# Optimization experiments

Measured on AMD Instinct MI355X. Metric: run time of the kernel, lower is better.

Reference implementation:

```python
import jax, jax.numpy as jnp
import numpy as np

H = 1024
V = 50257
S = 20


def setup_inputs() -> dict:
    key = jax.random.key(0)
    ks = jax.random.split(key, 13)
    sc = 0.02
    return {
        "token": jax.random.randint(ks[0], (1,), 0, V),
        "hidden": jax.random.normal(ks[1], (1, 1, H), jnp.float32),
        "encoder_outputs": jax.random.normal(ks[2], (S, 1, H), jnp.float32),
        "embed_table": jax.random.normal(ks[3], (V, H), jnp.float32) * sc,
        "attn_w": jax.random.normal(ks[4], (H, 2 * H), jnp.float32) * sc,
        "attn_b": jax.random.normal(ks[5], (H,), jnp.float32) * sc,
        "v_w": jax.random.normal(ks[6], (1, H), jnp.float32) * sc,
        "gru_w_ih": jax.random.normal(ks[7], (3 * H, 2 * H), jnp.float32) * sc,
        "gru_w_hh": jax.random.normal(ks[8], (3 * H, H), jnp.float32) * sc,
        "gru_b_ih": jax.random.normal(ks[9], (3 * H,), jnp.float32) * sc,
        "gru_b_hh": jax.random.normal(ks[10], (3 * H,), jnp.float32) * sc,
        "out_w": jax.random.normal(ks[11], (V, H), jnp.float32) * sc,
        "out_b": jax.random.normal(ks[12], (V,), jnp.float32) * sc,
    }


def reference(token, hidden, encoder_outputs, embed_table, attn_w, attn_b, v_w,
              gru_w_ih, gru_w_hh, gru_b_ih, gru_b_hh, out_w, out_b):
    s = encoder_outputs.shape[0]
    # embedding lookup -> [1,1,H]
    embed = embed_table[token].reshape(1, 1, -1)
    enc = jnp.transpose(encoder_outputs, (1, 0, 2))  # [1,S,H]
    h_rep = jnp.broadcast_to(hidden, (1, s, hidden.shape[-1]))  # repeat over src_len
    # Bahdanau additive attention
    energy = jnp.tanh(jnp.concatenate([h_rep, enc], axis=2) @ attn_w.T + attn_b)  # [1,S,H]
    scores = jnp.squeeze(energy @ v_w.T, axis=2)  # [1,S]
    attn = jax.nn.softmax(scores, axis=1)[:, None, :]  # [1,1,S]
    weighted = jnp.einsum('bqs,bsh->bqh', attn, enc)  # [1,1,H]
    # single-step GRU (PyTorch gate layout: r,z,n)
    x = jnp.concatenate([embed, weighted], axis=2)[0]  # [1,2H]
    h0 = hidden[0]  # [1,H]
    gi = x @ gru_w_ih.T + gru_b_ih  # [1,3H]
    gh = h0 @ gru_w_hh.T + gru_b_hh  # [1,3H]
    i_r, i_z, i_n = jnp.split(gi, 3, axis=1)
    h_r, h_z, h_n = jnp.split(gh, 3, axis=1)
    r = jax.nn.sigmoid(i_r + h_r)
    z = jax.nn.sigmoid(i_z + h_z)
    n = jnp.tanh(i_n + r * h_n)
    h_new = (1.0 - z) * n + z * h0  # [1,H]
    prediction = jax.nn.log_softmax(h_new @ out_w.T + out_b, axis=1)  # [1,V]
    return prediction, h_new[None]  # ([1,V], [1,1,H])
```

## Files before the change

### kernel.cpp

```cpp
#include <hip/hip_runtime.h>
#include <math.h>

#define H 1024
#define S 20
#define V 50257
#define NGRP ((V + 3) / 4)
#define KC_BLOCKS 512
#define KC_WAVES (KC_BLOCKS * 8)

__device__ __forceinline__ float wave_reduce_sum(float v) {
  #pragma unroll
  for (int off = 32; off > 0; off >>= 1)
    v += __shfl_xor(v, off, 64);
  return v;
}

__global__ __launch_bounds__(256) void kA(
    const int* __restrict__ token,
    const float* __restrict__ hidden,
    const float* __restrict__ enc,
    const float* __restrict__ embed_table,
    const float* __restrict__ attn_w,
    const float* __restrict__ attn_b,
    const float* __restrict__ v_w,
    const float* __restrict__ w_ih,
    const float* __restrict__ w_hh,
    const float* __restrict__ b_ih,
    const float* __restrict__ b_hh,
    float* __restrict__ bpart,
    float* __restrict__ gie,
    float* __restrict__ Emat,
    float* __restrict__ ghv)
{
  __shared__ float esh[4][S];
  const int t = threadIdx.x;
  const int lane = t & 63;
  const int wv = t >> 6;
  const int b = blockIdx.x;

  if (b < 256) {
    const int j = b * 4 + wv;
    const float* wrow = attn_w + (size_t)j * (2 * H);
    float4 wlo[4], whi[4], hid4[4];
    #pragma unroll
    for (int q = 0; q < 4; ++q) {
      const int idx = lane + 64 * q;
      wlo[q]  = ((const float4*)wrow)[idx];
      whi[q]  = ((const float4*)(wrow + H))[idx];
      hid4[q] = ((const float4*)hidden)[idx];
    }
    float hp = 0.f;
    #pragma unroll
    for (int q = 0; q < 4; ++q)
      hp += wlo[q].x * hid4[q].x + wlo[q].y * hid4[q].y +
            wlo[q].z * hid4[q].z + wlo[q].w * hid4[q].w;
    hp = wave_reduce_sum(hp);

    float myval = 0.f;
    #pragma unroll
    for (int s = 0; s < S; ++s) {
      const float4* e4 = (const float4*)(enc + s * H);
      float es = 0.f;
      #pragma unroll
      for (int q = 0; q < 4; ++q) {
        const float4 e = e4[lane + 64 * q];
        es += whi[q].x * e.x + whi[q].y * e.y + whi[q].z * e.z + whi[q].w * e.w;
      }
      es = wave_reduce_sum(es);
      if (lane == s) myval = es;
    }
    if (lane < S)
      esh[wv][lane] = tanhf(hp + myval + attn_b[j]) * v_w[j];
    __syncthreads();
    if (wv == 0 && lane < S)
      bpart[lane * 256 + b] =
          esh[0][lane] + esh[1][lane] + esh[2][lane] + esh[3][lane];
  } else if (b < 1024) {
    const int W = (b - 256) * 4 + wv;
    const float* wr = w_ih + (size_t)W * (2 * H);
    const float* embed = embed_table + (size_t)(*token) * H;
    float a = 0.f;
    #pragma unroll
    for (int q = 0; q < 4; ++q) {
      const int idx = lane + 64 * q;
      const float4 w = ((const float4*)wr)[idx];
      const float4 e = ((const float4*)embed)[idx];
      a += w.x * e.x + w.y * e.y + w.z * e.z + w.w * e.w;
    }
    a = wave_reduce_sum(a);
    if (lane == 0) gie[W] = a + b_ih[W];
  } else if (b < 1792) {
    const int W = (b - 1024) * 4 + wv;
    const float* wr = w_ih + (size_t)W * (2 * H) + H;
    float4 wv4[4];
    #pragma unroll
    for (int q = 0; q < 4; ++q) wv4[q] = ((const float4*)wr)[lane + 64 * q];
    float myE = 0.f;
    #pragma unroll
    for (int s = 0; s < S; ++s) {
      const float4* e4 = (const float4*)(enc + s * H);
      float es = 0.f;
      #pragma unroll
      for (int q = 0; q < 4; ++q) {
        const float4 e = e4[lane + 64 * q];
        es += wv4[q].x * e.x + wv4[q].y * e.y + wv4[q].z * e.z + wv4[q].w * e.w;
      }
      es = wave_reduce_sum(es);
      if (lane == s) myE = es;
    }
    if (lane < S) Emat[lane * (3 * H) + W] = myE;
  } else {
    const int W = (b - 1792) * 4 + wv;
    const float* wr = w_hh + (size_t)W * H;
    float a = 0.f;
    #pragma unroll
    for (int q = 0; q < 4; ++q) {
      const int idx = lane + 64 * q;
      const float4 w = ((const float4*)wr)[idx];
      const float4 h = ((const float4*)hidden)[idx];
      a += w.x * h.x + w.y * h.y + w.z * h.z + w.w * h.w;
    }
    a = wave_reduce_sum(a);
    if (lane == 0) ghv[W] = a + b_hh[W];
  }
}

__global__ __launch_bounds__(512) void kC(
    const float* __restrict__ bpart,
    const float* __restrict__ gie,
    const float* __restrict__ Emat,
    const float* __restrict__ ghv,
    const float* __restrict__ hidden,
    const float* __restrict__ out_w,
    const float* __restrict__ out_b,
    float* __restrict__ out,
    float* __restrict__ pmax,
    float* __restrict__ psum)
{
  __shared__ float scores_sh[S];
  __shared__ float attn_sh[S];
  __shared__ float hnew_lds[H];
  __shared__ float stat_m[8];
  __shared__ float stat_s[8];
  const int t = threadIdx.x;
  const int lane = t & 63;
  const int wv = t >> 6;
  const int b = blockIdx.x;

  for (int s = wv; s < S; s += 8) {
    const float4 p = ((const float4*)(bpart + s * 256))[lane];
    float v = wave_reduce_sum(p.x + p.y + p.z + p.w);
    if (lane == 0) scores_sh[s] = v;
  }
  __syncthreads();
  if (t == 0) {
    float m = -1e30f;
    for (int s = 0; s < S; ++s) m = fmaxf(m, scores_sh[s]);
    float sum = 0.f;
    for (int s = 0; s < S; ++s) {
      const float e = expf(scores_sh[s] - m);
      attn_sh[s] = e;
      sum += e;
    }
    const float inv = 1.f / sum;
    for (int s = 0; s < S; ++s) attn_sh[s] *= inv;
  }
  __syncthreads();

  #pragma unroll
  for (int r = 0; r < 2; ++r) {
    const int j = t + r * 512;
    float g0 = 0.f, g1 = 0.f, g2 = 0.f;
    #pragma unroll
    for (int s = 0; s < S; ++s) {
      const float a = attn_sh[s];
      const float* Es = Emat + s * (3 * H);
      g0 += a * Es[j];
      g1 += a * Es[H + j];
      g2 += a * Es[2 * H + j];
    }
    const float i_r = gie[j]         + g0;
    const float i_z = gie[H + j]     + g1;
    const float i_n = gie[2 * H + j] + g2;
    const float h_r = ghv[j];
    const float h_z = ghv[H + j];
    const float h_n = ghv[2 * H + j];
    const float rr = 1.f / (1.f + expf(-(i_r + h_r)));
    const float zz = 1.f / (1.f + expf(-(i_z + h_z)));
    const float nn = tanhf(i_n + rr * h_n);
    const float hn = (1.f - zz) * nn + zz * hidden[j];
    hnew_lds[j] = hn;
    if (b == 0) out[V + j] = hn;
  }
  __syncthreads();

  float4 h4[4];
  #pragma unroll
  for (int q = 0; q < 4; ++q)
    h4[q] = ((const float4*)hnew_lds)[lane + 64 * q];

  const int gw = b * 8 + wv;
  float wm = -INFINITY, wsum = 0.f;

  for (int grp = gw; grp < NGRP; grp += KC_WAVES) {
    const int vbase = grp * 4;
    const int v0 = vbase;
    const int v1 = (vbase + 1 < V) ? vbase + 1 : (V - 1);
    const int v2 = (vbase + 2 < V) ? vbase + 2 : (V - 1);
    const int v3 = (vbase + 3 < V) ? vbase + 3 : (V - 1);
    const float4* r0 = (const float4*)(out_w + (size_t)v0 * H);
    const float4* r1 = (const float4*)(out_w + (size_t)v1 * H);
    const float4* r2 = (const float4*)(out_w + (size_t)v2 * H);
    const float4* r3 = (const float4*)(out_w + (size_t)v3 * H);
    float a0 = 0.f, a1 = 0.f, a2 = 0.f, a3 = 0.f;
    #pragma unroll
    for (int q = 0; q < 4; ++q) {
      const int idx = lane + 64 * q;
      const float4 w0 = r0[idx];
      const float4 w1 = r1[idx];
      const float4 w2 = r2[idx];
      const float4 w3 = r3[idx];
      a0 += w0.x * h4[q].x + w0.y * h4[q].y + w0.z * h4[q].z + w0.w * h4[q].w;
      a1 += w1.x * h4[q].x + w1.y * h4[q].y + w1.z * h4[q].z + w1.w * h4[q].w;
      a2 += w2.x * h4[q].x + w2.y * h4[q].y + w2.z * h4[q].z + w2.w * h4[q].w;
      a3 += w3.x * h4[q].x + w3.y * h4[q].y + w3.z * h4[q].z + w3.w * h4[q].w;
    }
    a0 = wave_reduce_sum(a0);
    a1 = wave_reduce_sum(a1);
    a2 = wave_reduce_sum(a2);
    a3 = wave_reduce_sum(a3);
    const float val0 = a0 + out_b[v0];
    const float val1 = (vbase + 1 < V) ? a1 + out_b[v1] : -INFINITY;
    const float val2 = (vbase + 2 < V) ? a2 + out_b[v2] : -INFINITY;
    const float val3 = (vbase + 3 < V) ? a3 + out_b[v3] : -INFINITY;

    if (lane == 0) {
      if (vbase + 3 < V) {
        float4 o; o.x = val0; o.y = val1; o.z = val2; o.w = val3;
        *reinterpret_cast<float4*>(out + vbase) = o;
      } else {
        out[vbase] = val0;
        if (vbase + 1 < V) out[vbase + 1] = val1;
        if (vbase + 2 < V) out[vbase + 2] = val2;
      }
    }

    const float gm = fmaxf(fmaxf(val0, val1), fmaxf(val2, val3));
    const float M2 = fmaxf(wm, gm);
    wsum = wsum * expf(wm - M2) +
           expf(val0 - M2) + expf(val1 - M2) + expf(val2 - M2) + expf(val3 - M2);
    wm = M2;
  }

  if (lane == 0) { stat_m[wv] = wm; stat_s[wv] = wsum; }
  __syncthreads();
  if (t == 0) {
    float M = stat_m[0], Ss = stat_s[0];
    #pragma unroll
    for (int i = 1; i < 8; ++i) {
      const float m2 = stat_m[i], s2 = stat_s[i];
      const float M2 = fmaxf(M, m2);
      Ss = Ss * expf(M - M2) + s2 * expf(m2 - M2);
      M = M2;
    }
    pmax[b] = M;
    psum[b] = Ss;
  }
}

__global__ __launch_bounds__(512) void kD(
    const float* __restrict__ pmax,
    const float* __restrict__ psum,
    float* __restrict__ out)
{
  __shared__ float sm[8];
  __shared__ float ss[8];
  __shared__ float Tsh;
  const int t = threadIdx.x, lane = t & 63, wv = t >> 6;

  float dm = pmax[t];
  float dsv = psum[t];
  #pragma unroll
  for (int off = 32; off > 0; off >>= 1) {
    const float m2 = __shfl_xor(dm, off, 64);
    const float s2 = __shfl_xor(dsv, off, 64);
    const float M2 = fmaxf(dm, m2);
    dsv = dsv * expf(dm - M2) + s2 * expf(m2 - M2);
    dm = M2;
  }
  if (lane == 0) { sm[wv] = dm; ss[wv] = dsv; }
  __syncthreads();
  if (t == 0) {
    float M = sm[0], Ss = ss[0];
    #pragma unroll
    for (int i = 1; i < 8; ++i) {
      const float m2 = sm[i], s2 = ss[i];
      const float M2 = fmaxf(M, m2);
      Ss = Ss * expf(M - M2) + s2 * expf(m2 - M2);
      M = M2;
    }
    Tsh = M + logf(Ss);
  }
  __syncthreads();
  const float T = Tsh;
  const int i = blockIdx.x * 512 + t;
  if (i < V) out[i] -= T;
}

extern "C" void kernel_launch(void* const* d_in, const int* in_sizes, int n_in,
                              void* d_out, int out_size, void* d_ws, size_t ws_size,
                              hipStream_t stream) {
  const int*   token       = (const int*)d_in[0];
  const float* hidden      = (const float*)d_in[1];
  const float* enc         = (const float*)d_in[2];
  const float* embed_table = (const float*)d_in[3];
  const float* attn_w      = (const float*)d_in[4];
  const float* attn_b      = (const float*)d_in[5];
  const float* v_w         = (const float*)d_in[6];
  const float* w_ih        = (const float*)d_in[7];
  const float* w_hh        = (const float*)d_in[8];
  const float* b_ih        = (const float*)d_in[9];
  const float* b_hh        = (const float*)d_in[10];
  const float* out_w       = (const float*)d_in[11];
  const float* out_b       = (const float*)d_in[12];
  float* out = (float*)d_out;
  float* ws  = (float*)d_ws;

  float* bpart = ws;
  float* gie   = ws + 5120;
  float* ghv   = ws + 8192;
  float* Emat  = ws + 11264;
  float* pmax  = ws + 72704;
  float* psum  = ws + 73216;

  kA<<<2560, 256, 0, stream>>>(token, hidden, enc, embed_table, attn_w, attn_b,
                               v_w, w_ih, w_hh, b_ih, b_hh, bpart, gie, Emat, ghv);
  kC<<<KC_BLOCKS, 512, 0, stream>>>(bpart, gie, Emat, ghv, hidden,
                                    out_w, out_b, out, pmax, psum);
  kD<<<(V + 511) / 512, 512, 0, stream>>>(pmax, psum, out);
}
```

Measured before the change: 64.75 us.

## Split GRU cell into own kernel and give output-projection waves contiguous row ranges

Moves the attention softmax and GRU gate computation out of the vocab-projection kernel into a small 2-block kernel that writes h_new to workspace, so the 512 projection blocks no longer each redundantly recompute it. The projection kernel now assigns each wave a contiguous range of vocab rows instead of a strided interleave, and uses nontemporal loads for the streamed out_w rows. This adds an extra kernel launch and a global round trip for h_new in exchange for removing per-block redundant GRU work and improving streaming locality.

```diff
diff --git a/kernel.cpp b/kernel.cpp
--- a/kernel.cpp
+++ b/kernel.cpp
@@ -4,9 +4,10 @@
 #define H 1024
 #define S 20
 #define V 50257
-#define NGRP ((V + 3) / 4)
 #define KC_BLOCKS 512
 #define KC_WAVES (KC_BLOCKS * 8)
+
+typedef float v4f __attribute__((ext_vector_type(4)));
 
 __device__ __forceinline__ float wave_reduce_sum(float v) {
   #pragma unroll
@@ -125,27 +126,21 @@
   }
 }
 
-__global__ __launch_bounds__(512) void kC(
+__global__ __launch_bounds__(512) void kB2(
     const float* __restrict__ bpart,
     const float* __restrict__ gie,
     const float* __restrict__ Emat,
     const float* __restrict__ ghv,
     const float* __restrict__ hidden,
-    const float* __restrict__ out_w,
-    const float* __restrict__ out_b,
-    float* __restrict__ out,
-    float* __restrict__ pmax,
-    float* __restrict__ psum)
+    float* __restrict__ hnew,
+    float* __restrict__ out)
 {
   __shared__ float scores_sh[S];
   __shared__ float attn_sh[S];
-  __shared__ float hnew_lds[H];
-  __shared__ float stat_m[8];
-  __shared__ float stat_s[8];
   const int t = threadIdx.x;
   const int lane = t & 63;
   const int wv = t >> 6;
-  const int b = blockIdx.x;
+  const int j = blockIdx.x * 512 + t;
 
   for (int s = wv; s < S; s += 8) {
     const float4 p = ((const float4*)(bpart + s * 256))[lane];
@@ -167,59 +162,69 @@
   }
   __syncthreads();
 
+  float g0 = 0.f, g1 = 0.f, g2 = 0.f;
   #pragma unroll
-  for (int r = 0; r < 2; ++r) {
-    const int j = t + r * 512;
-    float g0 = 0.f, g1 = 0.f, g2 = 0.f;
-    #pragma unroll
-    for (int s = 0; s < S; ++s) {
-      const float a = attn_sh[s];
-      const float* Es = Emat + s * (3 * H);
-      g0 += a * Es[j];
-      g1 += a * Es[H + j];
-      g2 += a * Es[2 * H + j];
-    }
-    const float i_r = gie[j]         + g0;
-    const float i_z = gie[H + j]     + g1;
-    const float i_n = gie[2 * H + j] + g2;
-    const float h_r = ghv[j];
-    const float h_z = ghv[H + j];
-    const float h_n = ghv[2 * H + j];
-    const float rr = 1.f / (1.f + expf(-(i_r + h_r)));
-    const float zz = 1.f / (1.f + expf(-(i_z + h_z)));
-    const float nn = tanhf(i_n + rr * h_n);
-    const float hn = (1.f - zz) * nn + zz * hidden[j];
-    hnew_lds[j] = hn;
-    if (b == 0) out[V + j] = hn;
-  }
-  __syncthreads();
+  for (int s = 0; s < S; ++s) {
+    const float a = attn_sh[s];
+    const float* Es = Emat + s * (3 * H);
+    g0 += a * Es[j];
+    g1 += a * Es[H + j];
+    g2 += a * Es[2 * H + j];
+  }
+  const float i_r = gie[j]         + g0;
+  const float i_z = gie[H + j]     + g1;
+  const float i_n = gie[2 * H + j] + g2;
+  const float h_r = ghv[j];
+  const float h_z = ghv[H + j];
+  const float h_n = ghv[2 * H + j];
+  const float rr = 1.f / (1.f + expf(-(i_r + h_r)));
+  const float zz = 1.f / (1.f + expf(-(i_z + h_z)));
+  const float nn = tanhf(i_n + rr * h_n);
+  const float hn = (1.f - zz) * nn + zz * hidden[j];
+  hnew[j] = hn;
+  out[V + j] = hn;
+}
+
+__global__ __launch_bounds__(512, 4) void kC(
+    const float* __restrict__ hnew,
+    const float* __restrict__ out_w,
+    const float* __restrict__ out_b,
+    float* __restrict__ out,
+    float* __restrict__ pmax,
+    float* __restrict__ psum)
+{
+  __shared__ float stat_m[8];
+  __shared__ float stat_s[8];
+  const int t = threadIdx.x;
+  const int lane = t & 63;
+  const int wv = t >> 6;
+  const int b = blockIdx.x;
+  const long long gw = b * 8 + wv;
 
   float4 h4[4];
   #pragma unroll
   for (int q = 0; q < 4; ++q)
-    h4[q] = ((const float4*)hnew_lds)[lane + 64 * q];
-
-  const int gw = b * 8 + wv;
+    h4[q] = ((const float4*)hnew)[lane + 64 * q];
+
+  const int r0 = (int)((gw * V) / KC_WAVES);
+  const int r1 = (int)(((gw + 1) * V) / KC_WAVES);
+
   float wm = -INFINITY, wsum = 0.f;
 
-  for (int grp = gw; grp < NGRP; grp += KC_WAVES) {
-    const int vbase = grp * 4;
-    const int v0 = vbase;
-    const int v1 = (vbase + 1 < V) ? vbase + 1 : (V - 1);
-    const int v2 = (vbase + 2 < V) ? vbase + 2 : (V - 1);
-    const int v3 = (vbase + 3 < V) ? vbase + 3 : (V - 1);
-    const float4* r0 = (const float4*)(out_w + (size_t)v0 * H);
-    const float4* r1 = (const float4*)(out_w + (size_t)v1 * H);
-    const float4* r2 = (const float4*)(out_w + (size_t)v2 * H);
-    const float4* r3 = (const float4*)(out_w + (size_t)v3 * H);
+  int r = r0;
+  for (; r + 4 <= r1; r += 4) {
+    const v4f* p0 = (const v4f*)(out_w + (size_t)(r + 0) * H);
+    const v4f* p1 = (const v4f*)(out_w + (size_t)(r + 1) * H);
+    const v4f* p2 = (const v4f*)(out_w + (size_t)(r + 2) * H);
+    const v4f* p3 = (const v4f*)(out_w + (size_t)(r + 3) * H);
     float a0 = 0.f, a1 = 0.f, a2 = 0.f, a3 = 0.f;
     #pragma unroll
     for (int q = 0; q < 4; ++q) {
       const int idx = lane + 64 * q;
-      const float4 w0 = r0[idx];
-      const float4 w1 = r1[idx];
-      const float4 w2 = r2[idx];
-      const float4 w3 = r3[idx];
+      const v4f w0 = __builtin_nontemporal_load(p0 + idx);
+      const v4f w1 = __builtin_nontemporal_load(p1 + idx);
+      const v4f w2 = __builtin_nontemporal_load(p2 + idx);
+      const v4f w3 = __builtin_nontemporal_load(p3 + idx);
       a0 += w0.x * h4[q].x + w0.y * h4[q].y + w0.z * h4[q].z + w0.w * h4[q].w;
       a1 += w1.x * h4[q].x + w1.y * h4[q].y + w1.z * h4[q].z + w1.w * h4[q].w;
       a2 += w2.x * h4[q].x + w2.y * h4[q].y + w2.z * h4[q].z + w2.w * h4[q].w;
@@ -229,26 +234,34 @@
     a1 = wave_reduce_sum(a1);
     a2 = wave_reduce_sum(a2);
     a3 = wave_reduce_sum(a3);
-    const float val0 = a0 + out_b[v0];
-    const float val1 = (vbase + 1 < V) ? a1 + out_b[v1] : -INFINITY;
-    const float val2 = (vbase + 2 < V) ? a2 + out_b[v2] : -INFINITY;
-    const float val3 = (vbase + 3 < V) ? a3 + out_b[v3] : -INFINITY;
-
-    if (lane == 0) {
-      if (vbase + 3 < V) {
-        float4 o; o.x = val0; o.y = val1; o.z = val2; o.w = val3;
-        *reinterpret_cast<float4*>(out + vbase) = o;
-      } else {
-        out[vbase] = val0;
-        if (vbase + 1 < V) out[vbase + 1] = val1;
-        if (vbase + 2 < V) out[vbase + 2] = val2;
-      }
-    }
+    const float val0 = a0 + out_b[r + 0];
+    const float val1 = a1 + out_b[r + 1];
+    const float val2 = a2 + out_b[r + 2];
+    const float val3 = a3 + out_b[r + 3];
+
+    const float vv = (lane == 0) ? val0 : (lane == 1) ? val1
+                   : (lane == 2) ? val2 : val3;
+    if (lane < 4) out[r + lane] = vv;
 
     const float gm = fmaxf(fmaxf(val0, val1), fmaxf(val2, val3));
     const float M2 = fmaxf(wm, gm);
     wsum = wsum * expf(wm - M2) +
            expf(val0 - M2) + expf(val1 - M2) + expf(val2 - M2) + expf(val3 - M2);
+    wm = M2;
+  }
+  for (; r < r1; ++r) {
+    const v4f* p0 = (const v4f*)(out_w + (size_t)r * H);
+    float a0 = 0.f;
+    #pragma unroll
+    for (int q = 0; q < 4; ++q) {
+      const v4f w0 = __builtin_nontemporal_load(p0 + lane + 64 * q);
+      a0 += w0.x * h4[q].x + w0.y * h4[q].y + w0.z * h4[q].z + w0.w * h4[q].w;
+    }
+    a0 = wave_reduce_sum(a0);
+    const float val0 = a0 + out_b[r];
+    if (lane == 0) out[r] = val0;
+    const float M2 = fmaxf(wm, val0);
+    wsum = wsum * expf(wm - M2) + expf(val0 - M2);
     wm = M2;
   }
 
@@ -330,12 +343,13 @@
   float* gie   = ws + 5120;
   float* ghv   = ws + 8192;
   float* Emat  = ws + 11264;
-  float* pmax  = ws + 72704;
-  float* psum  = ws + 73216;
+  float* hnew  = ws + 72704;
+  float* pmax  = ws + 73728;
+  float* psum  = ws + 74240;
 
   kA<<<2560, 256, 0, stream>>>(token, hidden, enc, embed_table, attn_w, attn_b,
                                v_w, w_ih, w_hh, b_ih, b_hh, bpart, gie, Emat, ghv);
-  kC<<<KC_BLOCKS, 512, 0, stream>>>(bpart, gie, Emat, ghv, hidden,
-                                    out_w, out_b, out, pmax, psum);
+  kB2<<<2, 512, 0, stream>>>(bpart, gie, Emat, ghv, hidden, hnew, out);
+  kC<<<KC_BLOCKS, 512, 0, stream>>>(hnew, out_w, out_b, out, pmax, psum);
   kD<<<(V + 511) / 512, 512, 0, stream>>>(pmax, psum, out);
 }
```

New measurement: 65.81 us. Within noise of the previous version (+1.6%).
